# Kernel optimization log

Hardware: AMD Instinct MI355X
Metric: run time of the kernel (lower is better)

## Reference

```python
import jax, jax.numpy as jnp
import numpy as np

B, N, C, D = 128, 2000, 100, 128
H, DK = 8, 16
CLIP = 10.0
NEG = -1e9


def _unvisit_mean(emb, m):
    # emb: [B,N,D], m: [B,1,N] True = visited (zeroed); divide by N (faithful to source)
    return jnp.where(m[:, 0, :, None], 0.0, emb).sum(axis=1, keepdims=True) / emb.shape[1]


def setup_inputs() -> dict:
    key = jax.random.key(0)
    ks = jax.random.split(key, 16)
    f32 = jnp.float32
    return {
        'depot_embedding': jax.random.normal(ks[0], (B, 1, D), f32),
        'cluster_embedding': jax.random.normal(ks[1], (B, C, D), f32),
        'current_embedding': jax.random.normal(ks[2], (B, 1, D), f32),
        'node_embeddings': jax.random.normal(ks[3], (B, N, D), f32),
        'is_new_cluster': jax.random.bernoulli(ks[4], 0.5, (B,)),
        'cluster_mask': jax.random.bernoulli(ks[5], 0.3, (B, 1, N)),
        'visited_cluster_mask': jax.random.bernoulli(ks[6], 0.3, (B, 1, C)),
        'mask': jax.random.bernoulli(ks[7], 0.3, (B, 1, N)),
        'Wq': jax.random.normal(ks[8], (3 * D, D), f32) / np.float32(np.sqrt(3 * D)),
        'Wk': jax.random.normal(ks[9], (D, D), f32) / np.float32(np.sqrt(D)),
        'Wv': jax.random.normal(ks[10], (D, D), f32) / np.float32(np.sqrt(D)),
        'Wks': jax.random.normal(ks[11], (D, D), f32) / np.float32(np.sqrt(D)),
        'Wmq': jax.random.normal(ks[12], (D, H * DK), f32) / np.float32(np.sqrt(D)),
        'Wmk': jax.random.normal(ks[13], (D, H * DK), f32) / np.float32(np.sqrt(D)),
        'Wmv': jax.random.normal(ks[14], (D, H * DK), f32) / np.float32(np.sqrt(D)),
        'Wmo': jax.random.normal(ks[15], (H * DK, D), f32) / np.float32(np.sqrt(H * DK)),
    }


def reference(depot_embedding, cluster_embedding, current_embedding, node_embeddings,
              is_new_cluster, cluster_mask, visited_cluster_mask, mask,
              Wq, Wk, Wv, Wks, Wmq, Wmk, Wmv, Wmo):
    b, n, d = node_embeddings.shape
    c = cluster_embedding.shape[1]

    # masked mean-pool of unvisited nodes -> context [B,1,3D]
    unvisit_mean = _unvisit_mean(node_embeddings, mask)
    context = jnp.concatenate([unvisit_mean, current_embedding, depot_embedding], axis=2)
    q = context @ Wq                      # [B,1,D]
    k = cluster_embedding @ Wk            # [B,C,D]
    v = cluster_embedding @ Wv
    pk = cluster_embedding @ Wks

    # visited_cluster_mask[new, 0, 0] = ~all(visited[1:])  (scatter-update of mask)
    all_vis = jnp.all(visited_cluster_mask[:, 0, 1:], axis=1)          # [B]
    vcm0 = jnp.where(is_new_cluster, ~all_vis, visited_cluster_mask[:, 0, 0])
    vcm = visited_cluster_mask.at[:, 0, 0].set(vcm0)                   # [B,1,C]

    # masked MHA glimpse
    qh = (q @ Wmq).reshape(b, 1, H, DK).transpose(0, 2, 1, 3)          # [B,H,1,DK]
    kh = (k @ Wmk).reshape(b, c, H, DK).transpose(0, 2, 1, 3)          # [B,H,C,DK]
    vh = (v @ Wmv).reshape(b, c, H, DK).transpose(0, 2, 1, 3)
    scores = jnp.einsum('bhqk,bhck->bhqc', qh, kh) / jnp.sqrt(jnp.float32(DK))
    scores = jnp.where(vcm[:, None, :, :], NEG, scores)                # mask True -> -inf
    attn = jax.nn.softmax(scores, axis=-1)
    glimpse = jnp.einsum('bhqc,bhck->bhqk', attn, vh)                  # [B,H,1,DK]
    glimpse = glimpse.transpose(0, 2, 1, 3).reshape(b, 1, H * DK) @ Wmo  # [B,1,D]

    # tanh-clipped pointer logits over clusters
    logit = jnp.einsum('bqd,bcd->bqc', glimpse, pk)[:, 0, :] / jnp.sqrt(jnp.float32(d))
    logit = jnp.tanh(logit) * CLIP
    logit = jnp.where(vcm[:, 0, :], NEG, logit)
    log_p = jax.nn.log_softmax(logit, axis=1)                          # [B,C]

    guidance = jnp.argmax(log_p, axis=1)                               # greedy select
    guid_emb = jnp.take_along_axis(cluster_embedding, guidance[:, None, None], axis=1)  # [B,1,D]

    unvisit_cluster = _unvisit_mean(node_embeddings, mask | cluster_mask)
    aug = jnp.concatenate([unvisit_cluster, current_embedding, guid_emb, depot_embedding], axis=2)  # [B,1,4D]

    # scatter-combine: non-new batches keep step-0 init values (zeros)
    isn = is_new_cluster[:, None, None]
    aug = jnp.where(isn, aug, 0.0)
    guid_emb = jnp.where(isn, guid_emb, 0.0)
    guidance = jnp.where(is_new_cluster, guidance, 0).astype(jnp.int32)
    clu_prob = jnp.where(is_new_cluster[:, None], log_p, 0.0)
    return aug, guid_emb, guidance, clu_prob
```

## Files before the change

### kernel.cpp

```cpp
#include <hip/hip_runtime.h>
#include <math.h>

#define BB 128
#define NN 2000
#define CC 100
#define DD 128
#define NSPLIT 16
#define NEGV -1000000000.0f

#define OFF_P1   0
#define OFF_P2   (OFF_P1 + BB*NSPLIT*DD)
#define OFF_WQQ  (OFF_P2 + BB*NSPLIT*DD)
#define OFF_WKV  (OFF_WQQ + 384*DD)
#define OFF_SC   (OFF_WKV + DD*256)
#define OFF_VH   (OFF_SC + BB*8*CC)

#define OUT_AUG 0
#define OUT_GE  (BB*512)
#define OUT_GU  (OUT_GE + BB*DD)
#define OUT_CP  (OUT_GU + BB)

__global__ __launch_bounds__(256) void k_prep_sums(
    const float* __restrict__ node, const int* __restrict__ mask,
    const int* __restrict__ cmask, const int* __restrict__ is_new,
    const float* __restrict__ Wq, const float* __restrict__ Wmq,
    const float* __restrict__ Wk, const float* __restrict__ Wmk,
    const float* __restrict__ Wv, const float* __restrict__ Wmv,
    float* __restrict__ ws)
{
    int t = threadIdx.x;
    int blk = blockIdx.x;

    if (blk < 80) {
        const float *W1, *W2;
        float* wout; int rbase, ostride, ooff;
        if (blk < 48)      { W1 = Wq; W2 = Wmq; wout = ws + OFF_WQQ; rbase = blk*8;      ostride = 128; ooff = 0;   }
        else if (blk < 64) { W1 = Wk; W2 = Wmk; wout = ws + OFF_WKV; rbase = (blk-48)*8; ostride = 256; ooff = 0;   }
        else               { W1 = Wv; W2 = Wmv; wout = ws + OFF_WKV; rbase = (blk-64)*8; ostride = 256; ooff = 128; }
        int j = t & 127, r0 = t >> 7;
        float a0 = 0.f, a1 = 0.f, a2 = 0.f, a3 = 0.f;
        for (int k = 0; k < 128; k++) {
            float b2 = W2[k*128 + j];
            a0 += W1[(rbase + r0 + 0)*128 + k] * b2;
            a1 += W1[(rbase + r0 + 2)*128 + k] * b2;
            a2 += W1[(rbase + r0 + 4)*128 + k] * b2;
            a3 += W1[(rbase + r0 + 6)*128 + k] * b2;
        }
        wout[(rbase + r0 + 0)*ostride + ooff + j] = a0;
        wout[(rbase + r0 + 2)*ostride + ooff + j] = a1;
        wout[(rbase + r0 + 4)*ostride + ooff + j] = a2;
        wout[(rbase + r0 + 6)*ostride + ooff + j] = a3;
        return;
    }

    int idx = blk - 80;
    int b = idx >> 4, s = idx & 15;
    if (!is_new[b]) return;

    int lane = t & 31, q = t >> 5;
    float a1x=0,a1y=0,a1z=0,a1w=0, a2x=0,a2y=0,a2z=0,a2w=0;
    int n0 = s * 125;
    for (int r = q; r < 125; r += 8) {
        int n = n0 + r;
        if (mask[b*NN + n]) continue;
        const float4 x = *(const float4*)(node + ((size_t)b*NN + n)*DD + lane*4);
        a1x += x.x; a1y += x.y; a1z += x.z; a1w += x.w;
        if (!cmask[b*NN + n]) { a2x += x.x; a2y += x.y; a2z += x.z; a2w += x.w; }
    }
    __shared__ float s1[8][128];
    __shared__ float s2[8][128];
    s1[q][lane*4+0] = a1x; s1[q][lane*4+1] = a1y; s1[q][lane*4+2] = a1z; s1[q][lane*4+3] = a1w;
    s2[q][lane*4+0] = a2x; s2[q][lane*4+1] = a2y; s2[q][lane*4+2] = a2z; s2[q][lane*4+3] = a2w;
    __syncthreads();
    if (t < 128) {
        float v = 0.f;
        for (int qq = 0; qq < 8; qq++) v += s1[qq][t];
        ws[OFF_P1 + (b*NSPLIT + s)*DD + t] = v;
    } else {
        int d = t - 128;
        float v = 0.f;
        for (int qq = 0; qq < 8; qq++) v += s2[qq][d];
        ws[OFF_P2 + (b*NSPLIT + s)*DD + d] = v;
    }
}

__global__ __launch_bounds__(256) void k_cluster(
    const float* __restrict__ cluster, const float* __restrict__ current,
    const float* __restrict__ depot, const int* __restrict__ is_new,
    float* __restrict__ ws)
{
    int b = blockIdx.y;
    if (!is_new[b]) return;
    int t = threadIdx.x;
    const float* part1 = ws + OFF_P1;
    const float* Wqq   = ws + OFF_WQQ;
    const float* Wkv   = ws + OFF_WKV;
    float* scores      = ws + OFF_SC;
    float* vh          = ws + OFF_VH;

    __shared__ float ctx[384];
    __shared__ float qh_s[128];
    __shared__ float rowbuf[25*128];

    if (t < 128) {
        float v = 0.f;
        for (int s = 0; s < NSPLIT; s++) v += part1[(b*NSPLIT + s)*DD + t];
        ctx[t]       = v * (1.0f/2000.0f);
        ctx[256 + t] = depot[b*DD + t];
    } else {
        ctx[t] = current[b*DD + (t - 128)];
    }
    int base = blockIdx.x * 25;
    for (int idx = t; idx < 25*128; idx += 256)
        rowbuf[idx] = cluster[((size_t)b*CC + base + (idx >> 7))*DD + (idx & 127)];
    __syncthreads();

    if (t < 128) {
        float a = 0.f;
        for (int r = 0; r < 384; r++) a += ctx[r] * Wqq[r*128 + t];
        qh_s[t] = a;
    }
    __syncthreads();

    int g = t >> 6, l = t & 63;
    float acc[6][4];
    float acc6[4] = {0.f,0.f,0.f,0.f};
    #pragma unroll
    for (int m = 0; m < 6; m++) { acc[m][0]=0.f; acc[m][1]=0.f; acc[m][2]=0.f; acc[m][3]=0.f; }
    bool has7 = (g == 0);

    for (int i = 0; i < 128; i++) {
        float w0 = Wkv[i*256 +   0 + l];
        float w1 = Wkv[i*256 +  64 + l];
        float w2 = Wkv[i*256 + 128 + l];
        float w3 = Wkv[i*256 + 192 + l];
        #pragma unroll
        for (int m = 0; m < 6; m++) {
            float x = rowbuf[(g + 4*m)*128 + i];
            acc[m][0] += x*w0; acc[m][1] += x*w1; acc[m][2] += x*w2; acc[m][3] += x*w3;
        }
        if (has7) {
            float x = rowbuf[24*128 + i];
            acc6[0] += x*w0; acc6[1] += x*w1; acc6[2] += x*w2; acc6[3] += x*w3;
        }
    }

    #pragma unroll
    for (int m = 0; m < 7; m++) {
        int row = g + 4*m;
        if (row >= 25) break;
        float* a = (m < 6) ? acc[m] : acc6;
        int c = base + row;
        vh[((size_t)b*CC + c)*128 +      l] = a[2];
        vh[((size_t)b*CC + c)*128 + 64 + l] = a[3];
        float p0 = a[0] * qh_s[l];
        float p1 = a[1] * qh_s[64 + l];
        p0 += __shfl_xor(p0, 1); p0 += __shfl_xor(p0, 2); p0 += __shfl_xor(p0, 4); p0 += __shfl_xor(p0, 8);
        p1 += __shfl_xor(p1, 1); p1 += __shfl_xor(p1, 2); p1 += __shfl_xor(p1, 4); p1 += __shfl_xor(p1, 8);
        if ((l & 15) == 0) {
            scores[(b*8 +     (l >> 4))*CC + c] = p0 * 0.25f;
            scores[(b*8 + 4 + (l >> 4))*CC + c] = p1 * 0.25f;
        }
    }
}

__global__ __launch_bounds__(256) void k_final(
    const float* __restrict__ cluster, const float* __restrict__ current,
    const float* __restrict__ depot, const int* __restrict__ is_new,
    const int* __restrict__ visited, const float* __restrict__ Wks,
    const float* __restrict__ Wmo, float* __restrict__ ws,
    float* __restrict__ out)
{
    int b = blockIdx.x;
    int t = threadIdx.x;

    if (!is_new[b]) {
        for (int k = t; k < 512; k += 256) out[OUT_AUG + b*512 + k] = 0.f;
        if (t < 128) out[OUT_GE + b*DD + t] = 0.f;
        if (t == 0)  out[OUT_GU + b] = 0.f;
        if (t < 100) out[OUT_CP + b*CC + t] = 0.f;
        return;
    }

    const float* part2  = ws + OFF_P2;
    const float* scores = ws + OFF_SC;
    const float* vh     = ws + OFF_VH;

    __shared__ int   vcm_s[CC];
    __shared__ int   allv;
    __shared__ float attn[8][CC];
    __shared__ float gtmp[2][128];
    __shared__ float g_s[128], g1_s[128], g2_s[128];
    __shared__ float lg[CC];
    __shared__ int   g_idx;
    __shared__ float lse_s;

    if (t < CC) vcm_s[t] = (visited[b*CC + t] != 0);
    if (t == 0) allv = 1;
    __syncthreads();
    if (t >= 1 && t < CC && !vcm_s[t]) allv = 0;
    __syncthreads();
    if (t == 0) vcm_s[0] = allv ? 0 : 1;
    __syncthreads();

    {
        int h = t >> 5, l = t & 31;
        float smax = -1e30f;
        for (int c = l; c < CC; c += 32) {
            float v = scores[(b*8 + h)*CC + c];
            v = vcm_s[c] ? NEGV : v;
            attn[h][c] = v;
            smax = fmaxf(smax, v);
        }
        for (int o = 1; o < 32; o <<= 1) smax = fmaxf(smax, __shfl_xor(smax, o));
        float ssum = 0.f;
        for (int c = l; c < CC; c += 32) { float e = expf(attn[h][c] - smax); attn[h][c] = e; ssum += e; }
        for (int o = 1; o < 32; o <<= 1) ssum += __shfl_xor(ssum, o);
        float inv = 1.0f / ssum;
        for (int c = l; c < CC; c += 32) attn[h][c] *= inv;
    }
    __syncthreads();

    {
        int j = t & 127, half = t >> 7;
        float gacc = 0.f;
        for (int c = half*50; c < half*50 + 50; c++)
            gacc += attn[j >> 4][c] * vh[((size_t)b*CC + c)*128 + j];
        gtmp[half][j] = gacc;
    }
    __syncthreads();
    if (t < 128) g_s[t] = gtmp[0][t] + gtmp[1][t];
    __syncthreads();
    if (t < 128) {
        float a = 0.f;
        for (int i = 0; i < 128; i++) a += g_s[i] * Wmo[i*128 + t];
        g1_s[t] = a;
    }
    __syncthreads();
    if (t < 128) {
        float a = 0.f;
        for (int d = 0; d < 128; d++) a += Wks[t*128 + d] * g1_s[d];
        g2_s[t] = a * 0.08838834764831845f;
    }
    __syncthreads();
    if (t < 200) {
        int c = t >> 1, hf = t & 1;
        const float* cr = cluster + ((size_t)b*CC + c)*DD + hf*64;
        float a = 0.f;
        for (int i = 0; i < 64; i++) a += g2_s[hf*64 + i] * cr[i];
        a += __shfl_xor(a, 1);
        if (!hf) lg[c] = vcm_s[c] ? NEGV : 10.0f * tanhf(a);
    }
    __syncthreads();
    if (t < 32) {
        float bv = -1e30f; int bi = 0;
        for (int c = t; c < CC; c += 32) { float v = lg[c]; if (v > bv) { bv = v; bi = c; } }
        for (int o = 1; o < 32; o <<= 1) {
            float ov = __shfl_xor(bv, o); int oi = __shfl_xor(bi, o);
            if (ov > bv || (ov == bv && oi < bi)) { bv = ov; bi = oi; }
        }
        float se = 0.f;
        for (int c = t; c < CC; c += 32) se += expf(lg[c] - bv);
        for (int o = 1; o < 32; o <<= 1) se += __shfl_xor(se, o);
        if (t == 0) { g_idx = bi; lse_s = bv + logf(se); }
    }
    __syncthreads();

    int gi = g_idx; float lse = lse_s;
    if (t < CC)  out[OUT_CP + b*CC + t] = lg[t] - lse;
    if (t == 0)  out[OUT_GU + b] = (float)gi;
    if (t < 128) {
        float ge = cluster[((size_t)b*CC + gi)*DD + t];
        out[OUT_GE + b*DD + t] = ge;
        float uc = 0.f;
        for (int s = 0; s < NSPLIT; s++) uc += part2[(b*NSPLIT + s)*DD + t];
        out[OUT_AUG + b*512 +       t] = uc * (1.0f/2000.0f);
        out[OUT_AUG + b*512 + 128 + t] = current[b*DD + t];
        out[OUT_AUG + b*512 + 256 + t] = ge;
        out[OUT_AUG + b*512 + 384 + t] = depot[b*DD + t];
    }
}

extern "C" void kernel_launch(void* const* d_in, const int* in_sizes, int n_in,
                              void* d_out, int out_size, void* d_ws, size_t ws_size,
                              hipStream_t stream) {
    const float* depot   = (const float*)d_in[0];
    const float* cluster = (const float*)d_in[1];
    const float* current = (const float*)d_in[2];
    const float* node    = (const float*)d_in[3];
    const int*   is_new  = (const int*)d_in[4];
    const int*   cmask   = (const int*)d_in[5];
    const int*   visited = (const int*)d_in[6];
    const int*   mask    = (const int*)d_in[7];
    const float* Wq  = (const float*)d_in[8];
    const float* Wk  = (const float*)d_in[9];
    const float* Wv  = (const float*)d_in[10];
    const float* Wks = (const float*)d_in[11];
    const float* Wmq = (const float*)d_in[12];
    const float* Wmk = (const float*)d_in[13];
    const float* Wmv = (const float*)d_in[14];
    const float* Wmo = (const float*)d_in[15];
    float* ws  = (float*)d_ws;
    float* out = (float*)d_out;

    k_prep_sums<<<80 + BB*NSPLIT, 256, 0, stream>>>(node, mask, cmask, is_new,
                                                    Wq, Wmq, Wk, Wmk, Wv, Wmv, ws);
    k_cluster<<<dim3(4, BB), 256, 0, stream>>>(cluster, current, depot, is_new, ws);
    k_final<<<BB, 256, 0, stream>>>(cluster, current, depot, is_new, visited,
                                    Wks, Wmo, ws, out);
}
```

Measured before the change: 275.8 us.

## Fuse cluster and final kernels, reassociate attention to avoid K/V projections

Merges the cluster projection and final kernels into one per-batch kernel that stages the cluster embeddings in padded shared memory. Instead of projecting every cluster row through Wk/Wv, it folds the query into the key weights (u = Wk_h·q_h) and computes scores as cluster·u. It applies attention to the raw cluster rows before multiplying by the value weights. This removes the full K/V projection, the workspace round-trip for scores and values, and one launch. The cost is that only 128 blocks carry the whole stage, and each uses a large shared-memory allocation.

```diff
diff --git a/kernel.cpp b/kernel.cpp
--- a/kernel.cpp
+++ b/kernel.cpp
@@ -7,13 +7,12 @@
 #define DD 128
 #define NSPLIT 16
 #define NEGV -1000000000.0f
+#define CSTRIDE 129
 
 #define OFF_P1   0
 #define OFF_P2   (OFF_P1 + BB*NSPLIT*DD)
 #define OFF_WQQ  (OFF_P2 + BB*NSPLIT*DD)
 #define OFF_WKV  (OFF_WQQ + 384*DD)
-#define OFF_SC   (OFF_WKV + DD*256)
-#define OFF_VH   (OFF_SC + BB*8*CC)
 
 #define OUT_AUG 0
 #define OUT_GE  (BB*512)
@@ -84,23 +83,42 @@
     }
 }
 
-__global__ __launch_bounds__(256) void k_cluster(
+__global__ __launch_bounds__(256) void k_fused(
     const float* __restrict__ cluster, const float* __restrict__ current,
     const float* __restrict__ depot, const int* __restrict__ is_new,
-    float* __restrict__ ws)
+    const int* __restrict__ visited, const float* __restrict__ Wks,
+    const float* __restrict__ Wmo, const float* __restrict__ ws,
+    float* __restrict__ out)
 {
-    int b = blockIdx.y;
-    if (!is_new[b]) return;
+    int b = blockIdx.x;
     int t = threadIdx.x;
+
+    if (!is_new[b]) {
+        for (int k = t; k < 512; k += 256) out[OUT_AUG + b*512 + k] = 0.f;
+        if (t < 128) out[OUT_GE + b*DD + t] = 0.f;
+        if (t == 0)  out[OUT_GU + b] = 0.f;
+        if (t < 100) out[OUT_CP + b*CC + t] = 0.f;
+        return;
+    }
+
     const float* part1 = ws + OFF_P1;
+    const float* part2 = ws + OFF_P2;
     const float* Wqq   = ws + OFF_WQQ;
     const float* Wkv   = ws + OFF_WKV;
-    float* scores      = ws + OFF_SC;
-    float* vh          = ws + OFF_VH;
-
+
+    __shared__ float clu[CC*CSTRIDE];
     __shared__ float ctx[384];
+    __shared__ float qtmp[2][128];
     __shared__ float qh_s[128];
-    __shared__ float rowbuf[25*128];
+    __shared__ float uT[128*8];
+    __shared__ float sT[CC*9];
+    __shared__ float wS[8*128];
+    __shared__ float g_s[128], g1_s[128], g2_s[128];
+    __shared__ float lg[CC];
+    __shared__ int   vcm_s[CC];
+    __shared__ int   allv;
+    __shared__ int   g_idx;
+    __shared__ float lse_s;
 
     if (t < 128) {
         float v = 0.f;
@@ -110,126 +128,95 @@
     } else {
         ctx[t] = current[b*DD + (t - 128)];
     }
-    int base = blockIdx.x * 25;
-    for (int idx = t; idx < 25*128; idx += 256)
-        rowbuf[idx] = cluster[((size_t)b*CC + base + (idx >> 7))*DD + (idx & 127)];
-    __syncthreads();
-
-    if (t < 128) {
-        float a = 0.f;
-        for (int r = 0; r < 384; r++) a += ctx[r] * Wqq[r*128 + t];
-        qh_s[t] = a;
-    }
-    __syncthreads();
-
-    int g = t >> 6, l = t & 63;
-    float acc[6][4];
-    float acc6[4] = {0.f,0.f,0.f,0.f};
-    #pragma unroll
-    for (int m = 0; m < 6; m++) { acc[m][0]=0.f; acc[m][1]=0.f; acc[m][2]=0.f; acc[m][3]=0.f; }
-    bool has7 = (g == 0);
-
-    for (int i = 0; i < 128; i++) {
-        float w0 = Wkv[i*256 +   0 + l];
-        float w1 = Wkv[i*256 +  64 + l];
-        float w2 = Wkv[i*256 + 128 + l];
-        float w3 = Wkv[i*256 + 192 + l];
-        #pragma unroll
-        for (int m = 0; m < 6; m++) {
-            float x = rowbuf[(g + 4*m)*128 + i];
-            acc[m][0] += x*w0; acc[m][1] += x*w1; acc[m][2] += x*w2; acc[m][3] += x*w3;
-        }
-        if (has7) {
-            float x = rowbuf[24*128 + i];
-            acc6[0] += x*w0; acc6[1] += x*w1; acc6[2] += x*w2; acc6[3] += x*w3;
-        }
-    }
-
-    #pragma unroll
-    for (int m = 0; m < 7; m++) {
-        int row = g + 4*m;
-        if (row >= 25) break;
-        float* a = (m < 6) ? acc[m] : acc6;
-        int c = base + row;
-        vh[((size_t)b*CC + c)*128 +      l] = a[2];
-        vh[((size_t)b*CC + c)*128 + 64 + l] = a[3];
-        float p0 = a[0] * qh_s[l];
-        float p1 = a[1] * qh_s[64 + l];
-        p0 += __shfl_xor(p0, 1); p0 += __shfl_xor(p0, 2); p0 += __shfl_xor(p0, 4); p0 += __shfl_xor(p0, 8);
-        p1 += __shfl_xor(p1, 1); p1 += __shfl_xor(p1, 2); p1 += __shfl_xor(p1, 4); p1 += __shfl_xor(p1, 8);
-        if ((l & 15) == 0) {
-            scores[(b*8 +     (l >> 4))*CC + c] = p0 * 0.25f;
-            scores[(b*8 + 4 + (l >> 4))*CC + c] = p1 * 0.25f;
-        }
-    }
-}
-
-__global__ __launch_bounds__(256) void k_final(
-    const float* __restrict__ cluster, const float* __restrict__ current,
-    const float* __restrict__ depot, const int* __restrict__ is_new,
-    const int* __restrict__ visited, const float* __restrict__ Wks,
-    const float* __restrict__ Wmo, float* __restrict__ ws,
-    float* __restrict__ out)
-{
-    int b = blockIdx.x;
-    int t = threadIdx.x;
-
-    if (!is_new[b]) {
-        for (int k = t; k < 512; k += 256) out[OUT_AUG + b*512 + k] = 0.f;
-        if (t < 128) out[OUT_GE + b*DD + t] = 0.f;
-        if (t == 0)  out[OUT_GU + b] = 0.f;
-        if (t < 100) out[OUT_CP + b*CC + t] = 0.f;
-        return;
-    }
-
-    const float* part2  = ws + OFF_P2;
-    const float* scores = ws + OFF_SC;
-    const float* vh     = ws + OFF_VH;
-
-    __shared__ int   vcm_s[CC];
-    __shared__ int   allv;
-    __shared__ float attn[8][CC];
-    __shared__ float gtmp[2][128];
-    __shared__ float g_s[128], g1_s[128], g2_s[128];
-    __shared__ float lg[CC];
-    __shared__ int   g_idx;
-    __shared__ float lse_s;
-
     if (t < CC) vcm_s[t] = (visited[b*CC + t] != 0);
     if (t == 0) allv = 1;
+    for (int idx = t; idx < CC*DD; idx += 256)
+        clu[(idx >> 7)*CSTRIDE + (idx & 127)] = cluster[(size_t)b*CC*DD + idx];
     __syncthreads();
     if (t >= 1 && t < CC && !vcm_s[t]) allv = 0;
     __syncthreads();
     if (t == 0) vcm_s[0] = allv ? 0 : 1;
+
+    {
+        int j = t & 127, half = t >> 7;
+        float a = 0.f;
+        for (int r = half*192; r < half*192 + 192; r++) a += ctx[r] * Wqq[r*128 + j];
+        qtmp[half][j] = a;
+    }
+    __syncthreads();
+    if (t < 128) qh_s[t] = qtmp[0][t] + qtmp[1][t];
+    __syncthreads();
+
+    {
+        int i = t & 127, hq = t >> 7;
+        #pragma unroll
+        for (int hh = 0; hh < 4; hh++) {
+            int h = hq*4 + hh;
+            float a = 0.f;
+            #pragma unroll
+            for (int dk = 0; dk < 16; dk++)
+                a += Wkv[i*256 + h*16 + dk] * qh_s[h*16 + dk];
+            uT[i*8 + h] = a * 0.25f;
+        }
+    }
+    __syncthreads();
+
+    if (t < 200) {
+        int c = t >> 1, ih = t & 1;
+        float s0=0,s1=0,s2=0,s3=0,s4=0,s5=0,s6=0,s7=0;
+        for (int i = ih*64; i < ih*64 + 64; i++) {
+            float x = clu[c*CSTRIDE + i];
+            const float* u = &uT[i*8];
+            s0 += x*u[0]; s1 += x*u[1]; s2 += x*u[2]; s3 += x*u[3];
+            s4 += x*u[4]; s5 += x*u[5]; s6 += x*u[6]; s7 += x*u[7];
+        }
+        s0 += __shfl_xor(s0,1); s1 += __shfl_xor(s1,1); s2 += __shfl_xor(s2,1); s3 += __shfl_xor(s3,1);
+        s4 += __shfl_xor(s4,1); s5 += __shfl_xor(s5,1); s6 += __shfl_xor(s6,1); s7 += __shfl_xor(s7,1);
+        if (!ih) {
+            float* d = &sT[c*9];
+            d[0]=s0; d[1]=s1; d[2]=s2; d[3]=s3; d[4]=s4; d[5]=s5; d[6]=s6; d[7]=s7;
+        }
+    }
     __syncthreads();
 
     {
         int h = t >> 5, l = t & 31;
+        float vals[4]; int nv = 0;
         float smax = -1e30f;
         for (int c = l; c < CC; c += 32) {
-            float v = scores[(b*8 + h)*CC + c];
-            v = vcm_s[c] ? NEGV : v;
-            attn[h][c] = v;
+            float v = vcm_s[c] ? NEGV : sT[c*9 + h];
+            vals[nv++] = v;
             smax = fmaxf(smax, v);
         }
         for (int o = 1; o < 32; o <<= 1) smax = fmaxf(smax, __shfl_xor(smax, o));
-        float ssum = 0.f;
-        for (int c = l; c < CC; c += 32) { float e = expf(attn[h][c] - smax); attn[h][c] = e; ssum += e; }
+        float ssum = 0.f; nv = 0;
+        for (int c = l; c < CC; c += 32) { float e = expf(vals[nv] - smax); vals[nv++] = e; ssum += e; }
         for (int o = 1; o < 32; o <<= 1) ssum += __shfl_xor(ssum, o);
-        float inv = 1.0f / ssum;
-        for (int c = l; c < CC; c += 32) attn[h][c] *= inv;
-    }
-    __syncthreads();
-
-    {
-        int j = t & 127, half = t >> 7;
-        float gacc = 0.f;
-        for (int c = half*50; c < half*50 + 50; c++)
-            gacc += attn[j >> 4][c] * vh[((size_t)b*CC + c)*128 + j];
-        gtmp[half][j] = gacc;
-    }
-    __syncthreads();
-    if (t < 128) g_s[t] = gtmp[0][t] + gtmp[1][t];
+        float inv = 1.0f / ssum; nv = 0;
+        for (int c = l; c < CC; c += 32) sT[c*9 + h] = vals[nv++] * inv;
+    }
+    __syncthreads();
+
+    {
+        int i = t & 127, hq = t >> 7;
+        float a0=0,a1=0,a2=0,a3=0;
+        int h0 = hq*4;
+        for (int c = 0; c < CC; c++) {
+            float x = clu[c*CSTRIDE + i];
+            const float* at = &sT[c*9 + h0];
+            a0 += x*at[0]; a1 += x*at[1]; a2 += x*at[2]; a3 += x*at[3];
+        }
+        wS[(h0+0)*128 + i] = a0; wS[(h0+1)*128 + i] = a1;
+        wS[(h0+2)*128 + i] = a2; wS[(h0+3)*128 + i] = a3;
+    }
+    __syncthreads();
+
+    if (t < 128) {
+        int h = t >> 4;
+        float a = 0.f;
+        for (int i = 0; i < 128; i++) a += wS[h*128 + i] * Wkv[i*256 + 128 + t];
+        g_s[t] = a;
+    }
     __syncthreads();
     if (t < 128) {
         float a = 0.f;
@@ -239,17 +226,16 @@
     __syncthreads();
     if (t < 128) {
         float a = 0.f;
-        for (int d = 0; d < 128; d++) a += Wks[t*128 + d] * g1_s[d];
+        for (int e = 0; e < 128; e++) a += Wks[t*128 + e] * g1_s[e];
         g2_s[t] = a * 0.08838834764831845f;
     }
     __syncthreads();
     if (t < 200) {
-        int c = t >> 1, hf = t & 1;
-        const float* cr = cluster + ((size_t)b*CC + c)*DD + hf*64;
-        float a = 0.f;
-        for (int i = 0; i < 64; i++) a += g2_s[hf*64 + i] * cr[i];
+        int c = t >> 1, ih = t & 1;
+        float a = 0.f;
+        for (int i = ih*64; i < ih*64 + 64; i++) a += g2_s[i] * clu[c*CSTRIDE + i];
         a += __shfl_xor(a, 1);
-        if (!hf) lg[c] = vcm_s[c] ? NEGV : 10.0f * tanhf(a);
+        if (!ih) lg[c] = vcm_s[c] ? NEGV : 10.0f * tanhf(a);
     }
     __syncthreads();
     if (t < 32) {
@@ -270,7 +256,7 @@
     if (t < CC)  out[OUT_CP + b*CC + t] = lg[t] - lse;
     if (t == 0)  out[OUT_GU + b] = (float)gi;
     if (t < 128) {
-        float ge = cluster[((size_t)b*CC + gi)*DD + t];
+        float ge = clu[gi*CSTRIDE + t];
         out[OUT_GE + b*DD + t] = ge;
         float uc = 0.f;
         for (int s = 0; s < NSPLIT; s++) uc += part2[(b*NSPLIT + s)*DD + t];
@@ -305,7 +291,6 @@
 
     k_prep_sums<<<80 + BB*NSPLIT, 256, 0, stream>>>(node, mask, cmask, is_new,
                                                     Wq, Wmq, Wk, Wmk, Wv, Wmv, ws);
-    k_cluster<<<dim3(4, BB), 256, 0, stream>>>(cluster, current, depot, is_new, ws);
-    k_final<<<BB, 256, 0, stream>>>(cluster, current, depot, is_new, visited,
+    k_fused<<<BB, 256, 0, stream>>>(cluster, current, depot, is_new, visited,
                                     Wks, Wmo, ws, out);
 }
```

Result: faster. 242.9 us (median of 2 runs) (-11.9%).
